# Performance work log

Measured on AMD Instinct MI355X. Metric: run time of the kernel, lower is better.

The kernel has to match this reference:

```python
import jax, jax.numpy as jnp
import numpy as np

N_NODES = 100000
N_EDGES = 1600000
IN_CH = 128
HID = 64
HEADS = 4
N_GRAPHS = 64
NEG_SLOPE = 0.2
LN_EPS = 1e-5


def setup_inputs() -> dict:
    key = jax.random.key(0)
    ks = jax.random.split(key, 24)
    C1 = HID // HEADS  # 16 per-head channels for conv1
    inp = {
        "x": jax.random.normal(ks[0], (N_NODES, IN_CH), dtype=jnp.float32),
        "edge_index": jax.random.randint(ks[1], (2, N_EDGES), 0, N_NODES, dtype=jnp.int64),
        "batch": jnp.sort(jax.random.randint(ks[2], (N_NODES,), 0, N_GRAPHS, dtype=jnp.int64)),
        "num_graphs": N_GRAPHS,
        # conv1: GATConv(IN_CH -> C1, heads=HEADS, concat)
        "W1": jax.random.normal(ks[3], (IN_CH, HEADS * C1), dtype=jnp.float32) * 0.05,
        "att_src1": jax.random.normal(ks[4], (HEADS, C1), dtype=jnp.float32) * 0.1,
        "att_dst1": jax.random.normal(ks[5], (HEADS, C1), dtype=jnp.float32) * 0.1,
        "b1": jnp.zeros((HEADS * C1,), dtype=jnp.float32),
        # conv2: GATConv(HID -> HID, heads=1)
        "W2": jax.random.normal(ks[6], (HID, HID), dtype=jnp.float32) * 0.1,
        "att_src2": jax.random.normal(ks[7], (1, HID), dtype=jnp.float32) * 0.1,
        "att_dst2": jax.random.normal(ks[8], (1, HID), dtype=jnp.float32) * 0.1,
        "b2": jnp.zeros((HID,), dtype=jnp.float32),
        "ln_g": jnp.ones((HID,), dtype=jnp.float32),
        "ln_b": jnp.zeros((HID,), dtype=jnp.float32),
        "w_pool": jax.random.normal(ks[9], (HID, 1), dtype=jnp.float32) * 0.1,
        "b_pool": jnp.zeros((1,), dtype=jnp.float32),
        "w_fc1": jax.random.normal(ks[10], (HID, HID), dtype=jnp.float32) * 0.1,
        "b_fc1": jnp.zeros((HID,), dtype=jnp.float32),
        "w_fc2": jax.random.normal(ks[11], (HID, 1), dtype=jnp.float32) * 0.1,
        "b_fc2": jnp.zeros((1,), dtype=jnp.float32),
    }
    return inp


def gat_conv(x, src, dst, n_nodes, W, att_src, att_dst, bias, heads, out_ch):
    """PyG GATConv (add_self_loops already folded into src/dst)."""
    h = (x @ W).reshape(n_nodes, heads, out_ch)         # [N,H,C]
    a_s = jnp.sum(h * att_src[None], axis=-1)           # [N,H]
    a_d = jnp.sum(h * att_dst[None], axis=-1)           # [N,H]
    alpha = jax.nn.leaky_relu(a_s[src] + a_d[dst], NEG_SLOPE)  # [E,H]
    amax = jax.ops.segment_max(alpha, dst, num_segments=n_nodes)
    amax = jnp.where(jnp.isfinite(amax), amax, 0.0)
    ex = jnp.exp(alpha - amax[dst])
    denom = jax.ops.segment_sum(ex, dst, num_segments=n_nodes)
    w = ex / (denom[dst] + 1e-16)                       # segment softmax over in-edges
    msg = h[src] * w[:, :, None]                        # [E,H,C]
    out = jax.ops.segment_sum(msg, dst, num_segments=n_nodes)
    return out.reshape(n_nodes, heads * out_ch) + bias


def reference(x, edge_index, batch, num_graphs, W1, att_src1, att_dst1, b1,
              W2, att_src2, att_dst2, b2, ln_g, ln_b, w_pool, b_pool,
              w_fc1, b_fc1, w_fc2, b_fc2):
    n = x.shape[0]
    loop = jnp.arange(n, dtype=edge_index.dtype)
    src = jnp.concatenate([edge_index[0], loop])
    dst = jnp.concatenate([edge_index[1], loop])

    h = gat_conv(x, src, dst, n, W1, att_src1, att_dst1, b1, HEADS, HID // HEADS)
    h = jax.nn.elu(h)                                   # dropout is identity in eval
    h_res = h
    h = gat_conv(h, src, dst, n, W2, att_src2, att_dst2, b2, 1, HID)
    h = h + h_res
    mu = jnp.mean(h, axis=-1, keepdims=True)
    var = jnp.mean(jnp.square(h - mu), axis=-1, keepdims=True)
    h = (h - mu) / jnp.sqrt(var + LN_EPS) * ln_g + ln_b
    h = jax.nn.elu(h)

    attn = jax.nn.softmax(h @ w_pool + b_pool, axis=0)  # softmax over ALL nodes (dim=0)
    pooled = jax.ops.segment_sum(h * attn, batch, num_segments=num_graphs)  # [G,HID]
    z = jax.nn.elu(pooled @ w_fc1 + b_fc1)
    return z @ w_fc2 + b_fc2                            # [G,1]
```

## Files before the change

### kernel.cpp

```cpp
#include <hip/hip_runtime.h>
#include <math.h>

#define NN 100000
#define NE 1600000
#define ET (NE + NN)
#define ICH 128
#define HID 64
#define NGR 64
#define NB_SCAN 391

__device__ __forceinline__ float lrelu(float x){ return x > 0.f ? x : 0.2f*x; }
__device__ __forceinline__ float eluf(float x){ return x > 0.f ? x : expm1f(x); }

__device__ __forceinline__ float wsum64(float v){
  #pragma unroll
  for (int m = 32; m >= 1; m >>= 1) v += __shfl_xor(v, m);
  return v;
}
__device__ __forceinline__ float wsum16(float v){
  v += __shfl_xor(v, 8); v += __shfl_xor(v, 4);
  v += __shfl_xor(v, 2); v += __shfl_xor(v, 1);
  return v;
}
__device__ __forceinline__ int wscan_incl(int v){
  const int lane = threadIdx.x & 63;
  #pragma unroll
  for (int d = 1; d < 64; d <<= 1){
    int t = __shfl_up(v, d);
    if (lane >= d) v += t;
  }
  return v;
}

__global__ __launch_bounds__(256) void k_deg(const int* __restrict__ ei,
                                             int* __restrict__ deg)
{
  int e = blockIdx.x * 256 + threadIdx.x;
  if (e >= ET) return;
  int d = (e < NE) ? ei[NE + e] : (e - NE);
  atomicAdd(&deg[d], 1);
}

__global__ __launch_bounds__(256) void k_scanA(const int* __restrict__ deg,
    int* __restrict__ rowptr, int* __restrict__ bsum)
{
  int i = blockIdx.x * 256 + threadIdx.x;
  int v = (i < NN) ? deg[i] : 0;
  int incl = wscan_incl(v);
  __shared__ int wsums[4];
  int w = threadIdx.x >> 6, lane = threadIdx.x & 63;
  if (lane == 63) wsums[w] = incl;
  __syncthreads();
  int off = 0;
  for (int k = 0; k < w; ++k) off += wsums[k];
  if (i < NN) rowptr[i] = incl - v + off;
  if (threadIdx.x == 255) bsum[blockIdx.x] = off + incl;
}

__global__ __launch_bounds__(512) void k_scanB(const int* __restrict__ bsum,
                                               int* __restrict__ boff)
{
  int i = threadIdx.x;
  int v = (i < NB_SCAN) ? bsum[i] : 0;
  int incl = wscan_incl(v);
  __shared__ int wsums[8];
  int w = threadIdx.x >> 6, lane = threadIdx.x & 63;
  if (lane == 63) wsums[w] = incl;
  __syncthreads();
  int off = 0;
  for (int k = 0; k < w; ++k) off += wsums[k];
  if (i < NB_SCAN) boff[i] = incl - v + off;
}

__global__ __launch_bounds__(256) void k_scanC(int* __restrict__ rowptr,
    const int* __restrict__ boff, int* __restrict__ cursor)
{
  int i = blockIdx.x * 256 + threadIdx.x;
  if (i < NN){
    int val = rowptr[i] + boff[blockIdx.x];
    rowptr[i] = val;
    cursor[i] = val;
  }
  if (i == 0) rowptr[NN] = ET;
}

__global__ __launch_bounds__(256) void k_scatter(const int* __restrict__ ei,
    int* __restrict__ cursor, int* __restrict__ csr_src, int* __restrict__ csr_dst)
{
  int e = blockIdx.x * 256 + threadIdx.x;
  if (e >= ET) return;
  int s, d;
  if (e < NE){ s = ei[e]; d = ei[NE + e]; } else { s = d = e - NE; }
  int pos = atomicAdd(&cursor[d], 1);
  csr_src[pos] = s;
  csr_dst[pos] = d;
}

__global__ __launch_bounds__(256) void k_gemm1(const float* __restrict__ x,
    const float* __restrict__ W1, const float* __restrict__ asw,
    const float* __restrict__ adw, float* __restrict__ h1,
    float* __restrict__ as1, float* __restrict__ ad1)
{
  const int lane = threadIdx.x & 63;
  const int wid  = (blockIdx.x * 256 + threadIdx.x) >> 6;
  const int n0   = __builtin_amdgcn_readfirstlane(wid * 4);
  const float* xr = x + (size_t)n0 * ICH;
  float a0 = 0.f, a1 = 0.f, a2 = 0.f, a3 = 0.f;
  #pragma unroll 4
  for (int k = 0; k < ICH; ++k){
    const float w = W1[k * HID + lane];
    a0 = fmaf(xr[k],          w, a0);
    a1 = fmaf(xr[ICH + k],    w, a1);
    a2 = fmaf(xr[2*ICH + k],  w, a2);
    a3 = fmaf(xr[3*ICH + k],  w, a3);
  }
  const float sw = asw[lane], dw = adw[lane];
  float acc[4] = {a0, a1, a2, a3};
  #pragma unroll
  for (int i = 0; i < 4; ++i){
    const int n = n0 + i;
    h1[(size_t)n * HID + lane] = acc[i];
    float ps = wsum16(acc[i] * sw);
    float pd = wsum16(acc[i] * dw);
    if ((lane & 15) == 0){
      as1[n * 4 + (lane >> 4)] = ps;
      ad1[n * 4 + (lane >> 4)] = pd;
    }
  }
}

__global__ __launch_bounds__(256) void k_att1(const int* __restrict__ csr_src,
    const int* __restrict__ csr_dst, const float4* __restrict__ as1,
    const float4* __restrict__ ad1, float4* __restrict__ ex1)
{
  int i = blockIdx.x * 256 + threadIdx.x;
  if (i >= ET) return;
  float4 a = as1[csr_src[i]], b = ad1[csr_dst[i]];
  float4 E;
  E.x = expf(lrelu(a.x + b.x));
  E.y = expf(lrelu(a.y + b.y));
  E.z = expf(lrelu(a.z + b.z));
  E.w = expf(lrelu(a.w + b.w));
  ex1[i] = E;
}

__global__ __launch_bounds__(256) void k_conv1(const int* __restrict__ rowptr,
    const int* __restrict__ csr_src, const float* __restrict__ exf,
    const float* __restrict__ h1, const float* __restrict__ b1,
    float* __restrict__ hb)
{
  const int lane = threadIdx.x & 63;
  const int h = lane >> 4;
  const int n = (blockIdx.x * 256 + threadIdx.x) >> 6;
  const int row0 = __builtin_amdgcn_readfirstlane(rowptr[n]);
  const int row1 = __builtin_amdgcn_readfirstlane(rowptr[n + 1]);
  float acc = 0.f, den = 0.f;
  #pragma unroll 4
  for (int j = row0; j < row1; ++j){
    int s = csr_src[j];
    float eh = exf[(size_t)4 * j + h];
    den += eh;
    acc = fmaf(h1[(size_t)s * HID + lane], eh, acc);
  }
  float o = acc / (den + 1e-16f) + b1[lane];
  hb[(size_t)n * HID + lane] = eluf(o);
}

__global__ __launch_bounds__(256) void k_gemm2(const float* __restrict__ h,
    const float* __restrict__ W2, const float* __restrict__ asw,
    const float* __restrict__ adw, float* __restrict__ h2,
    float* __restrict__ as2, float* __restrict__ ad2)
{
  const int lane = threadIdx.x & 63;
  const int wid  = (blockIdx.x * 256 + threadIdx.x) >> 6;
  const int n0   = __builtin_amdgcn_readfirstlane(wid * 4);
  const float* hr = h + (size_t)n0 * HID;
  float a0 = 0.f, a1 = 0.f, a2 = 0.f, a3 = 0.f;
  #pragma unroll 4
  for (int k = 0; k < HID; ++k){
    const float w = W2[k * HID + lane];
    a0 = fmaf(hr[k],          w, a0);
    a1 = fmaf(hr[HID + k],    w, a1);
    a2 = fmaf(hr[2*HID + k],  w, a2);
    a3 = fmaf(hr[3*HID + k],  w, a3);
  }
  const float sw = asw[lane], dw = adw[lane];
  float acc[4] = {a0, a1, a2, a3};
  #pragma unroll
  for (int i = 0; i < 4; ++i){
    const int n = n0 + i;
    h2[(size_t)n * HID + lane] = acc[i];
    float ps = wsum64(acc[i] * sw);
    float pd = wsum64(acc[i] * dw);
    if (lane == 0){ as2[n] = ps; ad2[n] = pd; }
  }
}

__global__ __launch_bounds__(256) void k_att2(const int* __restrict__ csr_src,
    const int* __restrict__ csr_dst, const float* __restrict__ as2,
    const float* __restrict__ ad2, float* __restrict__ ex2)
{
  int i = blockIdx.x * 256 + threadIdx.x;
  if (i >= ET) return;
  ex2[i] = expf(lrelu(as2[csr_src[i]] + ad2[csr_dst[i]]));
}

__global__ __launch_bounds__(256) void k_conv2(const int* __restrict__ rowptr,
    const int* __restrict__ csr_src, const float* __restrict__ ex2,
    const float* __restrict__ h2, const float* __restrict__ b2,
    float* __restrict__ hb ,
    const float* __restrict__ lng, const float* __restrict__ lnb,
    const float* __restrict__ wpool, const float* __restrict__ bpool,
    float* __restrict__ es)
{
  const int lane = threadIdx.x & 63;
  const int n = (blockIdx.x * 256 + threadIdx.x) >> 6;
  const int row0 = __builtin_amdgcn_readfirstlane(rowptr[n]);
  const int row1 = __builtin_amdgcn_readfirstlane(rowptr[n + 1]);
  float acc = 0.f, den = 0.f;
  #pragma unroll 4
  for (int j = row0; j < row1; ++j){
    int s = csr_src[j];
    float e = ex2[j];
    den += e;
    acc = fmaf(h2[(size_t)s * HID + lane], e, acc);
  }
  const size_t idxn = (size_t)n * HID + lane;
  float t = acc / (den + 1e-16f) + b2[lane] + hb[idxn];
  float mu  = wsum64(t) * (1.f / 64.f);
  float dv  = t - mu;
  float var = wsum64(dv * dv) * (1.f / 64.f);
  float hv = dv * (1.f / sqrtf(var + 1e-5f)) * lng[lane] + lnb[lane];
  hv = eluf(hv);
  hb[idxn] = hv;
  float sl = wsum64(hv * wpool[lane]) + bpool[0];
  if (lane == 0) es[n] = expf(sl);
}

__global__ __launch_bounds__(256) void k_sumes(const float* __restrict__ es,
                                               float* __restrict__ S)
{
  float v = 0.f;
  for (int i = blockIdx.x * 256 + threadIdx.x; i < NN; i += gridDim.x * 256)
    v += es[i];
  v = wsum64(v);
  __shared__ float red[4];
  if ((threadIdx.x & 63) == 0) red[threadIdx.x >> 6] = v;
  __syncthreads();
  if (threadIdx.x == 0) atomicAdd(S, red[0] + red[1] + red[2] + red[3]);
}

__global__ __launch_bounds__(256) void k_pool(const float* __restrict__ hf,
    const float* __restrict__ es, const int* __restrict__ batch,
    const float* __restrict__ S, float* __restrict__ pooled)
{
  const int lane = threadIdx.x & 63;
  const int wseg = blockIdx.x * 4 + (threadIdx.x >> 6);
  const int base = wseg * 64;
  if (base >= NN) return;
  const float invS = 1.f / S[0];
  int end = base + 64; if (end > NN) end = NN;
  float acc = 0.f;
  int gprev = batch[base];
  for (int n = base; n < end; ++n){
    int g = batch[n];
    if (g != gprev){
      atomicAdd(&pooled[gprev * HID + lane], acc);
      acc = 0.f; gprev = g;
    }
    acc = fmaf(hf[(size_t)n * HID + lane], es[n] * invS, acc);
  }
  atomicAdd(&pooled[gprev * HID + lane], acc);
}

__global__ __launch_bounds__(64) void k_head(const float* __restrict__ pooled,
    const float* __restrict__ wfc1, const float* __restrict__ bfc1,
    const float* __restrict__ wfc2, const float* __restrict__ bfc2,
    float* __restrict__ out)
{
  const int g = blockIdx.x, j = threadIdx.x;
  const float* pr = pooled + g * HID;
  float acc = bfc1[j];
  #pragma unroll 4
  for (int k = 0; k < HID; ++k) acc = fmaf(pr[k], wfc1[k * HID + j], acc);
  float z = eluf(acc);
  float r = wsum64(z * wfc2[j]);
  if (j == 0) out[g] = r + bfc2[0];
}

extern "C" void kernel_launch(void* const* d_in, const int* in_sizes, int n_in,
                              void* d_out, int out_size, void* d_ws, size_t ws_size,
                              hipStream_t stream)
{
  const float* x     = (const float*)d_in[0];
  const int*   ei    = (const int*)d_in[1];
  const int*   batch = (const int*)d_in[2];
  const float* W1    = (const float*)d_in[4];
  const float* asw1  = (const float*)d_in[5];
  const float* adw1  = (const float*)d_in[6];
  const float* b1    = (const float*)d_in[7];
  const float* W2    = (const float*)d_in[8];
  const float* asw2  = (const float*)d_in[9];
  const float* adw2  = (const float*)d_in[10];
  const float* b2    = (const float*)d_in[11];
  const float* lng   = (const float*)d_in[12];
  const float* lnb   = (const float*)d_in[13];
  const float* wpool = (const float*)d_in[14];
  const float* bpool = (const float*)d_in[15];
  const float* wfc1  = (const float*)d_in[16];
  const float* bfc1  = (const float*)d_in[17];
  const float* wfc2  = (const float*)d_in[18];
  const float* bfc2  = (const float*)d_in[19];

  float* ws = (float*)d_ws;
  float* h1     = ws;
  float* hb     = ws +  6400000;
  float* ex1    = ws + 12800000;
  float* as1    = ws + 19600000;
  float* ad1    = ws + 20000000;
  float* as2    = ws + 20400000;
  float* ad2    = ws + 20500000;
  float* es     = ws + 20600000;
  float* pooled = ws + 20700000;
  float* Ssum   = ws + 20704096;
  int* iw       = (int*)(ws + 20704100);
  int* rowptr   = iw;
  int* cursor   = iw + 100004;
  int* deg      = iw + 200008;
  int* bsum     = iw + 300008;
  int* boff     = iw + 300520;
  int* csr_src  = iw + 301032;
  int* csr_dst  = iw + 2001032;

  hipMemsetAsync(deg, 0, (size_t)NN * 4, stream);
  hipMemsetAsync(pooled, 0, (size_t)NGR * 64 * 4, stream);
  hipMemsetAsync(Ssum, 0, 4, stream);

  k_deg    <<<(ET + 255) / 256, 256, 0, stream>>>(ei, deg);
  k_scanA  <<<NB_SCAN, 256, 0, stream>>>(deg, rowptr, bsum);
  k_scanB  <<<1, 512, 0, stream>>>(bsum, boff);
  k_scanC  <<<NB_SCAN, 256, 0, stream>>>(rowptr, boff, cursor);
  k_scatter<<<(ET + 255) / 256, 256, 0, stream>>>(ei, cursor, csr_src, csr_dst);

  k_gemm1<<<6250, 256, 0, stream>>>(x, W1, asw1, adw1, h1, as1, ad1);
  k_att1 <<<(ET + 255) / 256, 256, 0, stream>>>(csr_src, csr_dst,
                                                (const float4*)as1,
                                                (const float4*)ad1, (float4*)ex1);
  k_conv1<<<25000, 256, 0, stream>>>(rowptr, csr_src, ex1, h1, b1, hb);
  k_gemm2<<<6250, 256, 0, stream>>>(hb, W2, asw2, adw2, h1, as2, ad2);
  k_att2 <<<(ET + 255) / 256, 256, 0, stream>>>(csr_src, csr_dst, as2, ad2, ex1);
  k_conv2<<<25000, 256, 0, stream>>>(rowptr, csr_src, ex1, h1, b2, hb,
                                     lng, lnb, wpool, bpool, es);
  k_sumes<<<128, 256, 0, stream>>>(es, Ssum);
  k_pool <<<391, 256, 0, stream>>>(hb, es, batch, Ssum, pooled);
  k_head <<<64, 64, 0, stream>>>(pooled, wfc1, bfc1, wfc2, bfc2, (float*)d_out);
}
```

Baseline: 475.1 us.

## Fuse attention exp into aggregation and window CSR build by destination range

Removes the separate per-edge attention kernels and their edge-sized exp buffers. The conv kernels now recompute exp(leaky_relu(a_s[src]+a_d[dst])) inline, with the destination term hoisted per node and the self-loop handled outside the loop, so the CSR no longer stores self-loop entries or a dst array. Degree counting and scatter are partitioned into 8 destination windows, which is meant to keep the atomic targets L2-resident, at the cost of each block group rereading the full edge list. It also switches to fast __expf, which slightly changes accuracy, and the windowing makes the order of neighbours within each CSR row nondeterministic.

Measured after the change: 424.0 us. 10.8% less time.

```diff
diff --git a/kernel.cpp b/kernel.cpp
--- a/kernel.cpp
+++ b/kernel.cpp
@@ -3,11 +3,12 @@
 
 #define NN 100000
 #define NE 1600000
-#define ET (NE + NN)
 #define ICH 128
 #define HID 64
 #define NGR 64
 #define NB_SCAN 391
+#define NWIN 8
+#define WIN 12500
 
 __device__ __forceinline__ float lrelu(float x){ return x > 0.f ? x : 0.2f*x; }
 __device__ __forceinline__ float eluf(float x){ return x > 0.f ? x : expm1f(x); }
@@ -32,13 +33,15 @@
   return v;
 }
 
-__global__ __launch_bounds__(256) void k_deg(const int* __restrict__ ei,
+__global__ __launch_bounds__(256) void k_deg(const int* __restrict__ ei_dst,
                                              int* __restrict__ deg)
 {
-  int e = blockIdx.x * 256 + threadIdx.x;
-  if (e >= ET) return;
-  int d = (e < NE) ? ei[NE + e] : (e - NE);
-  atomicAdd(&deg[d], 1);
+  const int lo = (blockIdx.x & 7) * WIN, hi = lo + WIN;
+  const int nb = gridDim.x >> 3, ib = blockIdx.x >> 3;
+  for (int e = ib * 256 + threadIdx.x; e < NE; e += nb * 256){
+    int d = ei_dst[e];
+    if (d >= lo && d < hi) atomicAdd(&deg[d], 1);
+  }
 }
 
 __global__ __launch_bounds__(256) void k_scanA(const int* __restrict__ deg,
@@ -81,19 +84,21 @@
     rowptr[i] = val;
     cursor[i] = val;
   }
-  if (i == 0) rowptr[NN] = ET;
+  if (i == 0) rowptr[NN] = NE;
 }
 
 __global__ __launch_bounds__(256) void k_scatter(const int* __restrict__ ei,
-    int* __restrict__ cursor, int* __restrict__ csr_src, int* __restrict__ csr_dst)
-{
-  int e = blockIdx.x * 256 + threadIdx.x;
-  if (e >= ET) return;
-  int s, d;
-  if (e < NE){ s = ei[e]; d = ei[NE + e]; } else { s = d = e - NE; }
-  int pos = atomicAdd(&cursor[d], 1);
-  csr_src[pos] = s;
-  csr_dst[pos] = d;
+    int* __restrict__ cursor, int* __restrict__ csr_src)
+{
+  const int lo = (blockIdx.x & 7) * WIN, hi = lo + WIN;
+  const int nb = gridDim.x >> 3, ib = blockIdx.x >> 3;
+  for (int e = ib * 256 + threadIdx.x; e < NE; e += nb * 256){
+    int d = ei[NE + e];
+    if (d >= lo && d < hi){
+      int pos = atomicAdd(&cursor[d], 1);
+      csr_src[pos] = ei[e];
+    }
+  }
 }
 
 __global__ __launch_bounds__(256) void k_gemm1(const float* __restrict__ x,
@@ -129,38 +134,26 @@
   }
 }
 
-__global__ __launch_bounds__(256) void k_att1(const int* __restrict__ csr_src,
-    const int* __restrict__ csr_dst, const float4* __restrict__ as1,
-    const float4* __restrict__ ad1, float4* __restrict__ ex1)
-{
-  int i = blockIdx.x * 256 + threadIdx.x;
-  if (i >= ET) return;
-  float4 a = as1[csr_src[i]], b = ad1[csr_dst[i]];
-  float4 E;
-  E.x = expf(lrelu(a.x + b.x));
-  E.y = expf(lrelu(a.y + b.y));
-  E.z = expf(lrelu(a.z + b.z));
-  E.w = expf(lrelu(a.w + b.w));
-  ex1[i] = E;
-}
-
 __global__ __launch_bounds__(256) void k_conv1(const int* __restrict__ rowptr,
-    const int* __restrict__ csr_src, const float* __restrict__ exf,
-    const float* __restrict__ h1, const float* __restrict__ b1,
-    float* __restrict__ hb)
+    const int* __restrict__ csr_src, const float* __restrict__ as1,
+    const float* __restrict__ ad1, const float* __restrict__ h1,
+    const float* __restrict__ b1, float* __restrict__ hb)
 {
   const int lane = threadIdx.x & 63;
   const int h = lane >> 4;
   const int n = (blockIdx.x * 256 + threadIdx.x) >> 6;
   const int row0 = __builtin_amdgcn_readfirstlane(rowptr[n]);
   const int row1 = __builtin_amdgcn_readfirstlane(rowptr[n + 1]);
-  float acc = 0.f, den = 0.f;
+  const float adh = ad1[4 * n + h];
+  float eh = __expf(lrelu(as1[4 * n + h] + adh));
+  float den = eh;
+  float acc = eh * h1[(size_t)n * HID + lane];
   #pragma unroll 4
   for (int j = row0; j < row1; ++j){
     int s = csr_src[j];
-    float eh = exf[(size_t)4 * j + h];
-    den += eh;
-    acc = fmaf(h1[(size_t)s * HID + lane], eh, acc);
+    float e = __expf(lrelu(as1[4 * s + h] + adh));
+    den += e;
+    acc = fmaf(h1[(size_t)s * HID + lane], e, acc);
   }
   float o = acc / (den + 1e-16f) + b1[lane];
   hb[(size_t)n * HID + lane] = eluf(o);
@@ -196,19 +189,10 @@
   }
 }
 
-__global__ __launch_bounds__(256) void k_att2(const int* __restrict__ csr_src,
-    const int* __restrict__ csr_dst, const float* __restrict__ as2,
-    const float* __restrict__ ad2, float* __restrict__ ex2)
-{
-  int i = blockIdx.x * 256 + threadIdx.x;
-  if (i >= ET) return;
-  ex2[i] = expf(lrelu(as2[csr_src[i]] + ad2[csr_dst[i]]));
-}
-
 __global__ __launch_bounds__(256) void k_conv2(const int* __restrict__ rowptr,
-    const int* __restrict__ csr_src, const float* __restrict__ ex2,
-    const float* __restrict__ h2, const float* __restrict__ b2,
-    float* __restrict__ hb ,
+    const int* __restrict__ csr_src, const float* __restrict__ as2,
+    const float* __restrict__ ad2, const float* __restrict__ h2,
+    const float* __restrict__ b2, float* __restrict__ hb,
     const float* __restrict__ lng, const float* __restrict__ lnb,
     const float* __restrict__ wpool, const float* __restrict__ bpool,
     float* __restrict__ es)
@@ -217,11 +201,14 @@
   const int n = (blockIdx.x * 256 + threadIdx.x) >> 6;
   const int row0 = __builtin_amdgcn_readfirstlane(rowptr[n]);
   const int row1 = __builtin_amdgcn_readfirstlane(rowptr[n + 1]);
-  float acc = 0.f, den = 0.f;
+  const float adn = ad2[n];
+  float eh = __expf(lrelu(as2[n] + adn));
+  float den = eh;
+  float acc = eh * h2[(size_t)n * HID + lane];
   #pragma unroll 4
   for (int j = row0; j < row1; ++j){
     int s = csr_src[j];
-    float e = ex2[j];
+    float e = __expf(lrelu(as2[s] + adn));
     den += e;
     acc = fmaf(h2[(size_t)s * HID + lane], e, acc);
   }
@@ -234,7 +221,7 @@
   hv = eluf(hv);
   hb[idxn] = hv;
   float sl = wsum64(hv * wpool[lane]) + bpool[0];
-  if (lane == 0) es[n] = expf(sl);
+  if (lane == 0) es[n] = __expf(sl);
 }
 
 __global__ __launch_bounds__(256) void k_sumes(const float* __restrict__ es,
@@ -315,41 +302,35 @@
   float* ws = (float*)d_ws;
   float* h1     = ws;
   float* hb     = ws +  6400000;
-  float* ex1    = ws + 12800000;
-  float* as1    = ws + 19600000;
-  float* ad1    = ws + 20000000;
-  float* as2    = ws + 20400000;
-  float* ad2    = ws + 20500000;
-  float* es     = ws + 20600000;
-  float* pooled = ws + 20700000;
-  float* Ssum   = ws + 20704096;
-  int* iw       = (int*)(ws + 20704100);
+  float* as1    = ws + 12800000;
+  float* ad1    = ws + 13200000;
+  float* as2    = ws + 13600000;
+  float* ad2    = ws + 13700000;
+  float* es     = ws + 13800000;
+  float* pooled = ws + 13900000;
+  float* Ssum   = ws + 13904096;
+  int* iw       = (int*)(ws + 13904100);
   int* rowptr   = iw;
   int* cursor   = iw + 100004;
   int* deg      = iw + 200008;
   int* bsum     = iw + 300008;
   int* boff     = iw + 300520;
   int* csr_src  = iw + 301032;
-  int* csr_dst  = iw + 2001032;
 
   hipMemsetAsync(deg, 0, (size_t)NN * 4, stream);
   hipMemsetAsync(pooled, 0, (size_t)NGR * 64 * 4, stream);
   hipMemsetAsync(Ssum, 0, 4, stream);
 
-  k_deg    <<<(ET + 255) / 256, 256, 0, stream>>>(ei, deg);
+  k_deg    <<<2048, 256, 0, stream>>>(ei + NE, deg);
   k_scanA  <<<NB_SCAN, 256, 0, stream>>>(deg, rowptr, bsum);
   k_scanB  <<<1, 512, 0, stream>>>(bsum, boff);
   k_scanC  <<<NB_SCAN, 256, 0, stream>>>(rowptr, boff, cursor);
-  k_scatter<<<(ET + 255) / 256, 256, 0, stream>>>(ei, cursor, csr_src, csr_dst);
+  k_scatter<<<2048, 256, 0, stream>>>(ei, cursor, csr_src);
 
   k_gemm1<<<6250, 256, 0, stream>>>(x, W1, asw1, adw1, h1, as1, ad1);
-  k_att1 <<<(ET + 255) / 256, 256, 0, stream>>>(csr_src, csr_dst,
-                                                (const float4*)as1,
-                                                (const float4*)ad1, (float4*)ex1);
-  k_conv1<<<25000, 256, 0, stream>>>(rowptr, csr_src, ex1, h1, b1, hb);
+  k_conv1<<<25000, 256, 0, stream>>>(rowptr, csr_src, as1, ad1, h1, b1, hb);
   k_gemm2<<<6250, 256, 0, stream>>>(hb, W2, asw2, adw2, h1, as2, ad2);
-  k_att2 <<<(ET + 255) / 256, 256, 0, stream>>>(csr_src, csr_dst, as2, ad2, ex1);
-  k_conv2<<<25000, 256, 0, stream>>>(rowptr, csr_src, ex1, h1, b2, hb,
+  k_conv2<<<25000, 256, 0, stream>>>(rowptr, csr_src, as2, ad2, h1, b2, hb,
                                      lng, lnb, wpool, bpool, es);
   k_sumes<<<128, 256, 0, stream>>>(es, Ssum);
   k_pool <<<391, 256, 0, stream>>>(hb, es, batch, Ssum, pooled);
```
